# Kernel tuning notes

Hardware: AMD Instinct MI355X
Metric: run time of the kernel (lower is better)

Reference implementation:

```python
import jax, jax.numpy as jnp
import numpy as np

B, S, D, H, P, E, K, HID = 512, 32, 256, 4, 3, 8, 2, 1024


def setup_inputs() -> dict:
    key = jax.random.key(0)
    ks = jax.random.split(key, 24)
    g = lambda k, sh, sc=0.02: jax.random.normal(k, sh, jnp.float32) * sc
    return {
        'x': jax.random.normal(ks[0], (B, S, D), jnp.float32),
        'pos': jax.random.normal(ks[1], (B, S, P), jnp.float32),
        'ln1_w': jnp.ones((D,), jnp.float32), 'ln1_b': jnp.zeros((D,), jnp.float32),
        'ln2_w': jnp.ones((D,), jnp.float32), 'ln2_b': jnp.zeros((D,), jnp.float32),
        'q_w': g(ks[2], (D, D)), 'k_w': g(ks[3], (D, D)), 'v_w': g(ks[4], (D, D)),
        'p1_w': g(ks[5], (P, P), 0.3), 'p1_b': jnp.zeros((P,), jnp.float32),
        'p2_w': g(ks[6], (P, D // 8), 0.3), 'p2_b': jnp.zeros((D // 8,), jnp.float32),
        'head_w': g(ks[7], (D // 8, H), 0.1), 'head_b': jnp.zeros((H,), jnp.float32),
        'gate_p': jnp.ones((H,), jnp.float32),
        'out_w': g(ks[8], (D, D)), 'out_b': jnp.zeros((D,), jnp.float32),
        'w_gate': g(ks[9], (D, E), 0.1),
        'e_w1': g(ks[10], (E, D, HID)), 'e_b1': jnp.zeros((E, HID), jnp.float32),
        'e_w2': g(ks[11], (E, HID, D)), 'e_b2': jnp.zeros((E, D), jnp.float32),
    }


def _layer_norm(z, w, b):
    m = z.mean(-1, keepdims=True)
    v = ((z - m) ** 2).mean(-1, keepdims=True)
    return (z - m) * jax.lax.rsqrt(v + 1e-6) * w + b


def reference(x, pos, ln1_w, ln1_b, ln2_w, ln2_b, q_w, k_w, v_w,
              p1_w, p1_b, p2_w, p2_b, head_w, head_b, gate_p,
              out_w, out_b, w_gate, e_w1, e_b1, e_w2, e_b2):
    Bx, Sx, Dx = x.shape
    dh = Dx // H
    # --- gated attention (qk attn mixed with pos-relative attn) ---
    h = _layer_norm(x, ln1_w, ln1_b)
    q = (h @ q_w).reshape(Bx, Sx, H, dh).transpose(0, 2, 1, 3)
    k = (h @ k_w).reshape(Bx, Sx, H, dh).transpose(0, 2, 1, 3)
    v = (h @ v_w).reshape(Bx, Sx, H, dh).transpose(0, 2, 1, 3)
    attn = jax.nn.softmax(jnp.einsum('bhqd,bhkd->bhqk', q, k) / jnp.sqrt(jnp.float32(dh)), axis=-1)
    pf = jax.nn.relu(pos @ p1_w + p1_b) @ p2_w + p2_b          # [B,S,D//8]
    diff = pf[:, :, None, :] - pf[:, None, :, :]               # [B,S,S,D//8]
    pos_attn = jax.nn.softmax((diff @ head_w + head_b).transpose(0, 3, 1, 2), axis=-1)
    gsig = jax.nn.sigmoid(gate_p)[None, :, None, None]
    mix = (1.0 - gsig) * attn + gsig * pos_attn
    mix = mix / mix.sum(-1, keepdims=True)
    o = jnp.einsum('bhqk,bhkd->bhqd', mix, v).transpose(0, 2, 1, 3).reshape(Bx, Sx, Dx)
    x = x + (o @ out_w + out_b)
    # --- MoE FFN: noisy top-k gate (eval: no noise), dispatch, expert GEMM, combine ---
    h2 = _layer_norm(x, ln2_w, ln2_b)
    flat = h2.reshape(-1, Dx)                                   # [T,D]
    T = flat.shape[0]
    logits = flat @ w_gate                                      # [T,E]
    topv, topi = jax.lax.top_k(logits, K)
    gates = jax.nn.softmax(topv, axis=-1)                       # [T,K]
    C = 2 * T * K // E                                          # capacity factor 2 (effectively no drops)
    eidx = topi.reshape(-1)                                     # [T*K], token-major
    oh = jax.nn.one_hot(eidx, E, dtype=jnp.int32)
    posn = jnp.take_along_axis(jnp.cumsum(oh, axis=0) - 1, eidx[:, None], axis=1)[:, 0]
    keep = posn < C
    posc = jnp.where(keep, posn, 0)
    xd = jnp.repeat(flat, K, axis=0) * keep[:, None].astype(flat.dtype)
    buf = jnp.zeros((E, C, Dx), flat.dtype).at[eidx, posc].add(xd)   # grouped dispatch
    hh = jax.nn.gelu(jnp.einsum('ecd,edh->ech', buf, e_w1) + e_b1[:, None, :], approximate=False)
    y = jnp.einsum('ech,ehd->ecd', hh, e_w2) + e_b2[:, None, :]
    tok = y[eidx, posc] * (keep.astype(flat.dtype) * gates.reshape(-1))[:, None]
    moe_out = tok.reshape(T, K, Dx).sum(axis=1)
    return x + moe_out.reshape(Bx, Sx, Dx)
```

## Files before the change

### kernel.cpp

```cpp
#include <hip/hip_runtime.h>
#include <hip/hip_bf16.h>
#include <math.h>

#define BB 512
#define SS 32
#define DD 256
#define HH 4
#define DHH 64
#define PP 3
#define EE 8
#define KTOP 2
#define HID 1024
#define TT (BB*SS)
#define CAP 8192
#define TD ((size_t)TT*DD)

typedef short short8 __attribute__((ext_vector_type(8)));
typedef float f32x4 __attribute__((ext_vector_type(4)));

#define GLL(gp, lp) __builtin_amdgcn_global_load_lds( \
    (const __attribute__((address_space(1))) void*)(gp), \
    (__attribute__((address_space(3))) void*)(lp), 16, 0, 0)

__device__ __forceinline__ float wred(float v) {
#pragma unroll
  for (int off = 32; off; off >>= 1) v += __shfl_xor(v, off, 64);
  return v;
}

__device__ __forceinline__ float f4c(const float4& f, int u) {
  return (u == 0) ? f.x : (u == 1) ? f.y : (u == 2) ? f.z : f.w;
}

__device__ __forceinline__ unsigned short f2b(float f) {
  union { float f; unsigned u; } x; x.f = f;
  unsigned r = x.u + 0x7fffu + ((x.u >> 16) & 1u);
  return (unsigned short)(r >> 16);
}

__device__ __forceinline__ float b2f(unsigned short u) {
  union { unsigned u; float f; } x; x.u = ((unsigned)u) << 16;
  return x.f;
}

__device__ __forceinline__ unsigned cvt_pk_bf16(float lo, float hi) {
  unsigned r;
  asm("v_cvt_pk_bf16_f32 %0, %1, %2" : "=v"(r) : "v"(lo), "v"(hi));
  return r;
}

__device__ __forceinline__ float gelu_f(float x) {
  float x2 = x * x;
  float t2 = x * __builtin_fmaf(x2, 0.102943842f, 2.30212326f);
  float e = __builtin_amdgcn_exp2f(t2);
  float r = __builtin_amdgcn_rcpf(e + 1.f);
  float th = __builtin_fmaf(-2.f, r, 1.f);
  return 0.5f * x * (1.f + th);
}

__global__ void k_prep(
    const float* __restrict__ ew1, unsigned short* __restrict__ w1s,
    const float* __restrict__ ew2, unsigned short* __restrict__ w2s,
    const float* __restrict__ qw, const float* __restrict__ kw,
    const float* __restrict__ vw, unsigned short* __restrict__ wqkvf,
    const float* __restrict__ outw, unsigned short* __restrict__ woutf,
    const float* __restrict__ pos, const float* __restrict__ p1w,
    const float* __restrict__ p1b, const float* __restrict__ p2w,
    const float* __restrict__ p2b, const float* __restrict__ headw,
    float* __restrict__ pa,
    const float* __restrict__ x, const float* __restrict__ ln1w,
    const float* __restrict__ ln1b, unsigned short* __restrict__ rhi,
    unsigned short* __restrict__ rlo) {
  __shared__ float shbuf[2*HH*SS];
  int bid = blockIdx.x;
  int tid = threadIdx.x;
  if (bid < 2048) {
    const float* src = (bid < 1024) ? ew1 : ew2;
    unsigned short* dst = (bid < 1024) ? w1s : w2s;
    int K = (bid < 1024) ? DD : HID;
    int N = (bid < 1024) ? HID : DD;
    int idx = (bid & 1023) * 256 + tid;
    int lane = idx & 63;
    int tile = idx >> 6;
    int ntn = N >> 4;
    int ntk = K >> 5;
    int e = tile / (ntk * ntn);
    int rem = tile - e * (ntk * ntn);
    int kt = rem / ntn;
    int nt = rem - kt * ntn;
    int g = lane >> 4, c = lane & 15;
    const float* s = src + ((size_t)e * K + kt*32 + g*8) * N + nt*16 + c;
    short8 frag;
#pragma unroll
    for (int j = 0; j < 8; ++j) frag[j] = (short)f2b(s[(size_t)j * N]);
    reinterpret_cast<short8*>(dst)[(size_t)tile * 64 + lane] = frag;
  } else if (bid < 2144) {
    int tile = (bid - 2048) * 4 + (tid >> 6);
    int lane = tid & 63;
    int kt = tile / 48, nt = tile % 48;
    int c = lane & 15, g = lane >> 4;
    const float* W = (nt < 16) ? qw : (nt < 32) ? kw : vw;
    int col = (nt & 15) * 16 + c;
    const float* s = W + ((size_t)kt*32 + g*8)*DD + col;
    short8 hi, lo;
#pragma unroll
    for (int j = 0; j < 8; ++j) {
      float xx = s[(size_t)j * DD];
      unsigned short hb = f2b(xx);
      hi[j] = (short)hb;
      lo[j] = (short)f2b(xx - b2f(hb));
    }
    short8* d = reinterpret_cast<short8*>(wqkvf);
    d[(size_t)tile*128 + lane] = hi;
    d[(size_t)tile*128 + 64 + lane] = lo;
  } else if (bid < 2176) {
    int tile = (bid - 2144) * 4 + (tid >> 6);
    int lane = tid & 63;
    int kt = tile >> 4, nt = tile & 15;
    int c = lane & 15, g = lane >> 4;
    int col = nt * 16 + c;
    const float* s = outw + ((size_t)kt*32 + g*8)*DD + col;
    short8 hi, lo;
#pragma unroll
    for (int j = 0; j < 8; ++j) {
      float xx = s[(size_t)j * DD];
      unsigned short hb = f2b(xx);
      hi[j] = (short)hb;
      lo[j] = (short)f2b(xx - b2f(hb));
    }
    short8* d = reinterpret_cast<short8*>(woutf);
    d[(size_t)tile*128 + lane] = hi;
    d[(size_t)tile*128 + 64 + lane] = lo;
  } else if (bid < 2688) {
    int b = bid - 2176;
    float* ph = shbuf;
    float* ex = shbuf + HH*SS;
    if (tid < 128) {
      int s = tid >> 2, hd = tid & 3;
      const float* pp = pos + ((size_t)b * SS + s) * PP;
      float p0 = pp[0], p1 = pp[1], p2 = pp[2];
      float t0 = fmaxf(0.f, p0*p1w[0] + p1*p1w[3] + p2*p1w[6] + p1b[0]);
      float t1 = fmaxf(0.f, p0*p1w[1] + p1*p1w[4] + p2*p1w[7] + p1b[1]);
      float t2 = fmaxf(0.f, p0*p1w[2] + p1*p1w[5] + p2*p1w[8] + p1b[2]);
      float acc = 0.f;
#pragma unroll
      for (int c = 0; c < 32; ++c) {
        float pf = t0*p2w[c] + t1*p2w[32+c] + t2*p2w[64+c] + p2b[c];
        acc += pf * headw[c*4 + hd];
      }
      ph[hd*SS + s] = acc;
    }
    __syncthreads();
    if (tid < 4) {
      int h2 = tid;
      float mx = -1e30f;
      for (int j = 0; j < 32; ++j) mx = fmaxf(mx, -ph[h2*SS + j]);
      float sum = 0.f;
      for (int j = 0; j < 32; ++j) { float e = expf(-ph[h2*SS + j] - mx); ex[h2*SS + j] = e; sum += e; }
      float inv = 1.f / sum;
      for (int j = 0; j < 32; ++j) pa[((size_t)b*HH + h2)*SS + j] = ex[h2*SS + j] * inv;
    }
  } else {
    int t = (bid - 2688) * 4 + (tid >> 6);
    int lane = tid & 63;
    float4 xv = reinterpret_cast<const float4*>(x + (size_t)t * DD)[lane];
    float s1 = xv.x + xv.y + xv.z + xv.w;
    float s2 = xv.x*xv.x + xv.y*xv.y + xv.z*xv.z + xv.w*xv.w;
    s1 = wred(s1); s2 = wred(s2);
    float m = s1 * (1.f/256.f);
    float var = s2 * (1.f/256.f) - m*m;
    float rs = rsqrtf(var + 1e-6f);
    float4 wv = reinterpret_cast<const float4*>(ln1w)[lane];
    float4 bv = reinterpret_cast<const float4*>(ln1b)[lane];
    float4 o;
    o.x = (xv.x-m)*rs*wv.x + bv.x;
    o.y = (xv.y-m)*rs*wv.y + bv.y;
    o.z = (xv.z-m)*rs*wv.z + bv.z;
    o.w = (xv.w-m)*rs*wv.w + bv.w;
    ushort4 h4, l4;
    h4.x = f2b(o.x); l4.x = f2b(o.x - b2f(h4.x));
    h4.y = f2b(o.y); l4.y = f2b(o.y - b2f(h4.y));
    h4.z = f2b(o.z); l4.z = f2b(o.z - b2f(h4.z));
    h4.w = f2b(o.w); l4.w = f2b(o.w - b2f(h4.w));
    *reinterpret_cast<ushort4*>(rhi + (size_t)t * DD + lane*4) = h4;
    *reinterpret_cast<ushort4*>(rlo + (size_t)t * DD + lane*4) = l4;
  }
}

__global__ __launch_bounds__(512, 4) void k_qkvm(
    const unsigned short* __restrict__ hr, const unsigned short* __restrict__ lr,
    const unsigned short* __restrict__ wqkvf,
    float* __restrict__ q, float* __restrict__ k, float* __restrict__ v) {
  __shared__ short8 AF[2048];
  int tid = threadIdx.x, lane = tid & 63, w = tid >> 6;
  int c = lane & 15, g = lane >> 4;
#pragma unroll
  for (int i = 0; i < 4; ++i) {
    int comb = i*8 + w;
    int mt = comb >> 4, slot = comb & 15;
    int kt = slot & 7;
    const unsigned short* src = (slot < 8) ? hr : lr;
    const unsigned short* sp = src + ((size_t)(blockIdx.x*32 + mt*16 + c)*DD + kt*32 + g*8);
    GLL(sp, AF + comb*64);
  }
  const short8* wfv = reinterpret_cast<const short8*>(wqkvf);
  f32x4 acc[2][6] = {};
  __syncthreads();
#pragma unroll
  for (int kt = 0; kt < 8; ++kt) {
    short8 bh[6], bl[6];
#pragma unroll
    for (int n = 0; n < 6; ++n) {
      const short8* bp = wfv + ((size_t)kt*48 + w*6 + n)*128;
      bh[n] = bp[lane]; bl[n] = bp[64 + lane];
    }
    short8 ah[2], al[2];
#pragma unroll
    for (int mt = 0; mt < 2; ++mt) {
      ah[mt] = AF[(mt*16 + kt)*64 + lane];
      al[mt] = AF[(mt*16 + 8 + kt)*64 + lane];
    }
    __builtin_amdgcn_s_setprio(1);
#pragma unroll
    for (int n = 0; n < 6; ++n)
#pragma unroll
      for (int mt = 0; mt < 2; ++mt) {
        acc[mt][n] = __builtin_amdgcn_mfma_f32_16x16x32_bf16(ah[mt], bh[n], acc[mt][n], 0, 0, 0);
        acc[mt][n] = __builtin_amdgcn_mfma_f32_16x16x32_bf16(al[mt], bh[n], acc[mt][n], 0, 0, 0);
        acc[mt][n] = __builtin_amdgcn_mfma_f32_16x16x32_bf16(ah[mt], bl[n], acc[mt][n], 0, 0, 0);
      }
    __builtin_amdgcn_s_setprio(0);
  }
#pragma unroll
  for (int n = 0; n < 6; ++n) {
    int col = w*96 + n*16 + c;
    int wsel = col >> 8, cc = col & 255;
    int hd = cc >> 6, d2 = cc & 63;
    float* OUT = (wsel == 0) ? q : (wsel == 1) ? k : v;
#pragma unroll
    for (int mt = 0; mt < 2; ++mt) {
#pragma unroll
      for (int r = 0; r < 4; ++r) {
        int tok = (blockIdx.x*2 + mt)*16 + g*4 + r;
        int b = tok >> 5, s = tok & 31;
        OUT[(((size_t)b*HH + hd)*SS + s)*DHH + d2] = acc[mt][n][r];
      }
    }
  }
}

__global__ __launch_bounds__(512, 4) void k_outm(
    const unsigned short* __restrict__ hr, const unsigned short* __restrict__ lr,
    const unsigned short* __restrict__ wof,
    const float* __restrict__ xres, const float* __restrict__ bias,
    float* __restrict__ out) {
  __shared__ short8 AF[2048];
  int tid = threadIdx.x, lane = tid & 63, w = tid >> 6;
  int c = lane & 15, g = lane >> 4;
#pragma unroll
  for (int i = 0; i < 4; ++i) {
    int comb = i*8 + w;
    int mt = comb >> 4, slot = comb & 15;
    int kt = slot & 7;
    const unsigned short* src = (slot < 8) ? hr : lr;
    const unsigned short* sp = src + ((size_t)(blockIdx.x*32 + mt*16 + c)*DD + kt*32 + g*8);
    GLL(sp, AF + comb*64);
  }
  const short8* wfv = reinterpret_cast<const short8*>(wof);
  f32x4 acc[2][2] = {};
  __syncthreads();
#pragma unroll
  for (int kt = 0; kt < 8; ++kt) {
    short8 bh[2], bl[2];
#pragma unroll
    for (int n = 0; n < 2; ++n) {
      const short8* bp = wfv + ((size_t)kt*16 + w*2 + n)*128;
      bh[n] = bp[lane]; bl[n] = bp[64 + lane];
    }
    short8 ah[2], al[2];
#pragma unroll
    for (int mt = 0; mt < 2; ++mt) {
      ah[mt] = AF[(mt*16 + kt)*64 + lane];
      al[mt] = AF[(mt*16 + 8 + kt)*64 + lane];
    }
    __builtin_amdgcn_s_setprio(1);
#pragma unroll
    for (int n = 0; n < 2; ++n)
#pragma unroll
      for (int mt = 0; mt < 2; ++mt) {
        acc[mt][n] = __builtin_amdgcn_mfma_f32_16x16x32_bf16(ah[mt], bh[n], acc[mt][n], 0, 0, 0);
        acc[mt][n] = __builtin_amdgcn_mfma_f32_16x16x32_bf16(al[mt], bh[n], acc[mt][n], 0, 0, 0);
        acc[mt][n] = __builtin_amdgcn_mfma_f32_16x16x32_bf16(ah[mt], bl[n], acc[mt][n], 0, 0, 0);
      }
    __builtin_amdgcn_s_setprio(0);
  }
#pragma unroll
  for (int n = 0; n < 2; ++n) {
    int col = (w*2 + n)*16 + c;
    float bb = bias[col];
#pragma unroll
    for (int mt = 0; mt < 2; ++mt) {
#pragma unroll
      for (int r = 0; r < 4; ++r) {
        int tok = (blockIdx.x*2 + mt)*16 + g*4 + r;
        size_t idx = (size_t)tok*DD + col;
        out[idx] = xres[idx] + acc[mt][n][r] + bb;
      }
    }
  }
}

__global__ __launch_bounds__(256) void k_attn(const float* __restrict__ q, const float* __restrict__ k,
        const float* __restrict__ v, const float* __restrict__ pa, const float* __restrict__ gate_p,
        unsigned short* __restrict__ ahi, unsigned short* __restrict__ alo) {
  int bh = blockIdx.x;
  int b = bh >> 2, hd = bh & 3;
  __shared__ float qs[32][65];
  __shared__ float ks[32][65];
  __shared__ float vs[32][64];
  __shared__ float ssm[32][33];
  __shared__ float pas[32];
  int tid = threadIdx.x;
  const float* qb = q + (size_t)bh * (SS*DHH);
  const float* kb = k + (size_t)bh * (SS*DHH);
  const float* vb = v + (size_t)bh * (SS*DHH);
  for (int it = tid; it < 512; it += 256) {
    int row = it >> 4, col = (it & 15) * 4;
    float4 qv = *reinterpret_cast<const float4*>(qb + row*DHH + col);
    float4 kv = *reinterpret_cast<const float4*>(kb + row*DHH + col);
    float4 vv = *reinterpret_cast<const float4*>(vb + row*DHH + col);
    qs[row][col] = qv.x; qs[row][col+1] = qv.y; qs[row][col+2] = qv.z; qs[row][col+3] = qv.w;
    ks[row][col] = kv.x; ks[row][col+1] = kv.y; ks[row][col+2] = kv.z; ks[row][col+3] = kv.w;
    *reinterpret_cast<float4*>(&vs[row][col]) = vv;
  }
  if (tid < 32) pas[tid] = pa[(size_t)bh * SS + tid];
  __syncthreads();
#pragma unroll
  for (int rr = 0; rr < 4; ++rr) {
    int id = tid + 256*rr;
    int i = id >> 5, j = id & 31;
    float acc = 0.f;
#pragma unroll
    for (int d = 0; d < 64; ++d) acc += qs[i][d] * ks[j][d];
    ssm[i][j] = acc * 0.125f;
  }
  __syncthreads();
  float gs = 1.f / (1.f + expf(-gate_p[hd]));
  float ga = 1.f - gs;
  {
    int i = tid >> 3, sub = tid & 7;
    float v0 = ssm[i][sub*4+0], v1 = ssm[i][sub*4+1];
    float v2 = ssm[i][sub*4+2], v3 = ssm[i][sub*4+3];
    float mx = fmaxf(fmaxf(v0, v1), fmaxf(v2, v3));
#pragma unroll
    for (int off = 1; off < 8; off <<= 1) mx = fmaxf(mx, __shfl_xor(mx, off, 64));
    float e0 = expf(v0-mx), e1 = expf(v1-mx), e2 = expf(v2-mx), e3 = expf(v3-mx);
    float s = e0 + e1 + e2 + e3;
#pragma unroll
    for (int off = 1; off < 8; off <<= 1) s += __shfl_xor(s, off, 64);
    float inv = 1.f / s;
    ssm[i][sub*4+0] = ga*e0*inv + gs*pas[sub*4+0];
    ssm[i][sub*4+1] = ga*e1*inv + gs*pas[sub*4+1];
    ssm[i][sub*4+2] = ga*e2*inv + gs*pas[sub*4+2];
    ssm[i][sub*4+3] = ga*e3*inv + gs*pas[sub*4+3];
  }
  __syncthreads();
  {
    int w = tid >> 6, lane = tid & 63;
    int mt = w & 1, ktl = w >> 1;
    int c = lane & 15, g = lane >> 4;
    int tokl = mt*16 + c;
    int dbase = ktl*32 + g*8;
    float acc[8] = {};
#pragma unroll
    for (int j = 0; j < 32; ++j) {
      float s = ssm[tokl][j];
      float4 va = *reinterpret_cast<float4*>(&vs[j][dbase]);
      float4 vb2 = *reinterpret_cast<float4*>(&vs[j][dbase+4]);
      acc[0] += s*va.x;  acc[1] += s*va.y;  acc[2] += s*va.z;  acc[3] += s*va.w;
      acc[4] += s*vb2.x; acc[5] += s*vb2.y; acc[6] += s*vb2.z; acc[7] += s*vb2.w;
    }
    short8 hi, lo;
#pragma unroll
    for (int j = 0; j < 8; ++j) {
      unsigned short hb = f2b(acc[j]);
      hi[j] = (short)hb;
      lo[j] = (short)f2b(acc[j] - b2f(hb));
    }
    size_t base = ((size_t)(b*SS + tokl))*DD + hd*DHH + dbase;
    *reinterpret_cast<short8*>(ahi + base) = hi;
    *reinterpret_cast<short8*>(alo + base) = lo;
  }
}

__global__ void k_gate(const float* __restrict__ xo, const float* __restrict__ w,
                       const float* __restrict__ b, const float* __restrict__ wg,
                       unsigned short* __restrict__ flatb, int* __restrict__ topi,
                       float* __restrict__ gates) {
  int t = blockIdx.x * 4 + (threadIdx.x >> 6);
  int lane = threadIdx.x & 63;
  float4 xv = reinterpret_cast<const float4*>(xo + (size_t)t * DD)[lane];
  float s1 = xv.x + xv.y + xv.z + xv.w;
  float s2 = xv.x*xv.x + xv.y*xv.y + xv.z*xv.z + xv.w*xv.w;
  s1 = wred(s1); s2 = wred(s2);
  float m = s1 * (1.f/256.f);
  float var = s2 * (1.f/256.f) - m*m;
  float rs = rsqrtf(var + 1e-6f);
  float4 wv = reinterpret_cast<const float4*>(w)[lane];
  float4 bv = reinterpret_cast<const float4*>(b)[lane];
  float4 fv;
  fv.x = (xv.x-m)*rs*wv.x + bv.x;
  fv.y = (xv.y-m)*rs*wv.y + bv.y;
  fv.z = (xv.z-m)*rs*wv.z + bv.z;
  fv.w = (xv.w-m)*rs*wv.w + bv.w;
  ushort4 fb;
  fb.x = f2b(fv.x); fb.y = f2b(fv.y); fb.z = f2b(fv.z); fb.w = f2b(fv.w);
  *reinterpret_cast<ushort4*>(flatb + (size_t)t * DD + lane*4) = fb;
  float pe[8] = {};
  const float* wgp = wg + lane*4*EE;
#pragma unroll
  for (int dd = 0; dd < 4; ++dd) {
    float fd = f4c(fv, dd);
#pragma unroll
    for (int e2 = 0; e2 < 8; ++e2) pe[e2] += fd * wgp[dd*EE + e2];
  }
#pragma unroll
  for (int off = 32; off; off >>= 1) {
#pragma unroll
    for (int e2 = 0; e2 < 8; ++e2) pe[e2] += __shfl_xor(pe[e2], off, 64);
  }
  if (lane == 0) {
    float best = -1e30f, second = -1e30f; int bi = 0, si = 0;
#pragma unroll
    for (int e2 = 0; e2 < 8; ++e2) {
      float vv = pe[e2];
      if (vv > best) { second = best; si = bi; best = vv; bi = e2; }
      else if (vv > second) { second = vv; si = e2; }
    }
    float e1 = expf(second - best);
    float inv = 1.f / (1.f + e1);
    topi[t*2+0] = bi; topi[t*2+1] = si;
    gates[t*2+0] = inv; gates[t*2+1] = e1 * inv;
  }
}

__global__ void k_hist(const int* __restrict__ topi, int* __restrict__ bc) {
  __shared__ int cnt[EE];
  int tid = threadIdx.x;
  if (tid < EE) cnt[tid] = 0;
  __syncthreads();
  int e = topi[blockIdx.x*256 + tid];
  atomicAdd(&cnt[e], 1);
  __syncthreads();
  if (tid < EE) bc[blockIdx.x*EE + tid] = cnt[tid];
}

__global__ void k_disp(const int* __restrict__ topi, const int* __restrict__ bc,
                       int* __restrict__ ltok, int* __restrict__ slotof,
                       int* __restrict__ cnt) {
  __shared__ int offs[EE];
  __shared__ int wcnt[4][EE];
  int tid = threadIdx.x;
  {
    int e = tid >> 5, l32 = tid & 31;
    int sumP = 0, sumT = 0;
#pragma unroll
    for (int it = 0; it < 4; ++it) {
      int blk = l32 + it*32;
      int vv = bc[blk*EE + e];
      sumT += vv;
      if (blk < blockIdx.x) sumP += vv;
    }
#pragma unroll
    for (int off = 1; off < 32; off <<= 1) {
      sumP += __shfl_xor(sumP, off, 32);
      sumT += __shfl_xor(sumT, off, 32);
    }
    if (l32 == 0) {
      offs[e] = sumP;
      if (blockIdx.x == 0) cnt[e] = sumT;
    }
  }
  __syncthreads();
  int i = blockIdx.x*256 + tid;
  int e = topi[i];
  int wv = tid >> 6, lane = tid & 63;
  unsigned long long lt = (1ull << lane) - 1ull;
  int prefix = 0;
#pragma unroll
  for (int ee = 0; ee < EE; ++ee) {
    unsigned long long mb = __ballot(e == ee);
    if (e == ee) prefix = __popcll(mb & lt);
    if (lane == 0) wcnt[wv][ee] = __popcll(mb);
  }
  __syncthreads();
  int off = offs[e];
  for (int w2 = 0; w2 < wv; ++w2) off += wcnt[w2][e];
  int pos = off + prefix;
  if (pos < CAP) { ltok[e*CAP + pos] = i >> 1; slotof[i] = e*CAP + pos; }
  else           { slotof[i] = -1; }
}

__global__ __launch_bounds__(512, 4) void k_expert(
    const unsigned short* __restrict__ flatb, const unsigned short* __restrict__ w1s,
    const float* __restrict__ b1, const unsigned short* __restrict__ w2s,
    const float* __restrict__ b2,
    const int* __restrict__ ltok, const int* __restrict__ cnt,
    unsigned short* __restrict__ ybuf) {
  int e = blockIdx.x & 7;
  int rt0 = blockIdx.x >> 3;
  int kept = cnt[e]; if (kept > CAP) kept = CAP;
  int r0 = rt0 * 64;
  if (r0 >= kept) return;
  __shared__ short8 AsV[2048];
  __shared__ short8 H1V[2048];
  int tid = threadIdx.x;
  int lane = tid & 63;
  int w = tid >> 6;
  int c = lane & 15, g = lane >> 4;
  int ts = w & 1, dq = w >> 1;
  {
    const short8* fb = reinterpret_cast<const short8*>(flatb);
#pragma unroll
    for (int it = 0; it < 4; ++it) {
      int id = tid + it*512;
      int row = id >> 5, ch = id & 31;
      int rr = r0 + row;
      int src = (rr < kept) ? rr : r0;
      int tok = ltok[e*CAP + src];
      AsV[row*32 + (ch ^ (row & 7))] = fb[(size_t)tok*32 + ch];
    }
  }
  const short8* w1v = reinterpret_cast<const short8*>(w1s);
  const short8* w2v = reinterpret_cast<const short8*>(w2s);
  f32x4 y[2][4] = {};
  __syncthreads();
  for (int hc = 0; hc < 8; ++hc) {
    f32x4 hacc[4] = {};
    short8 wf[8];
#pragma unroll
    for (int kt = 0; kt < 8; ++kt)
      wf[kt] = w1v[((size_t)(e*8 + kt)*64 + hc*8 + w)*64 + lane];
#pragma unroll
    for (int kt = 0; kt < 8; ++kt) {
      __builtin_amdgcn_s_setprio(1);
#pragma unroll
      for (int ctT = 0; ctT < 4; ++ctT) {
        short8 a = AsV[(ctT*16 + c)*32 + ((kt*4 + g) ^ (c & 7))];
        hacc[ctT] = __builtin_amdgcn_mfma_f32_16x16x32_bf16(wf[kt], a, hacc[ctT], 0, 0, 0);
      }
      __builtin_amdgcn_s_setprio(0);
    }
    float4 b1v = *reinterpret_cast<const float4*>(b1 + e*HID + hc*128 + w*16 + g*4);
    {
      uint2* h1u = reinterpret_cast<uint2*>(H1V + (hc & 1)*1024);
#pragma unroll
      for (int ctT = 0; ctT < 4; ++ctT) {
        float v0 = gelu_f(hacc[ctT][0] + b1v.x);
        float v1 = gelu_f(hacc[ctT][1] + b1v.y);
        float v2 = gelu_f(hacc[ctT][2] + b1v.z);
        float v3 = gelu_f(hacc[ctT][3] + b1v.w);
        uint2 pk;
        pk.x = cvt_pk_bf16(v0, v1);
        pk.y = cvt_pk_bf16(v2, v3);
        int tok = ctT*16 + c;
        h1u[(tok*32 + w*4 + g) ^ ((c & 7) << 1)] = pk;
      }
    }
    __syncthreads();
#pragma unroll
    for (int hk = 0; hk < 4; ++hk) {
      short8 wg2[4];
#pragma unroll
      for (int ct = 0; ct < 4; ++ct)
        wg2[ct] = w2v[((size_t)(e*32 + hc*4 + hk)*16 + dq*4 + ct)*64 + lane];
      short8 a2[2];
#pragma unroll
      for (int rt = 0; rt < 2; ++rt) {
        int row = (ts*2 + rt)*16 + c;
        a2[rt] = H1V[(hc & 1)*1024 + row*16 + ((hk*4 + g) ^ (c & 7))];
      }
      __builtin_amdgcn_s_setprio(1);
#pragma unroll
      for (int ct = 0; ct < 4; ++ct)
#pragma unroll
        for (int rt = 0; rt < 2; ++rt)
          y[rt][ct] = __builtin_amdgcn_mfma_f32_16x16x32_bf16(a2[rt], wg2[ct], y[rt][ct], 0, 0, 0);
      __builtin_amdgcn_s_setprio(0);
    }
  }
  float bb2[4];
#pragma unroll
  for (int ct = 0; ct < 4; ++ct) bb2[ct] = b2[e*DD + (dq*4 + ct)*16 + c];
#pragma unroll
  for (int rt = 0; rt < 2; ++rt) {
#pragma unroll
    for (int q = 0; q < 4; ++q) {
      int tok = (ts*2 + rt)*16 + g*4 + q;
      if (r0 + tok < kept) {
        size_t base = (size_t)(e*CAP + r0 + tok) * DD;
#pragma unroll
        for (int ct = 0; ct < 4; ++ct) {
          int dd = (dq*4 + ct)*16 + c;
          ybuf[base + dd] = f2b(y[rt][ct][q] + bb2[ct]);
        }
      }
    }
  }
}

__global__ void k_comb(const unsigned short* __restrict__ ybuf, const int* __restrict__ slotof,
                       const float* __restrict__ gates, float* __restrict__ out) {
  int t = blockIdx.x * 4 + (threadIdx.x >> 6);
  int lane = threadIdx.x & 63;
  int s0 = slotof[t*2], s1 = slotof[t*2+1];
  float g0 = gates[t*2], g1 = gates[t*2+1];
  float4 o = reinterpret_cast<float4*>(out + (size_t)t*DD)[lane];
  if (s0 >= 0) {
    ushort4 a = reinterpret_cast<const ushort4*>(ybuf + (size_t)s0*DD)[lane];
    o.x += g0*b2f(a.x); o.y += g0*b2f(a.y); o.z += g0*b2f(a.z); o.w += g0*b2f(a.w);
  }
  if (s1 >= 0) {
    ushort4 a = reinterpret_cast<const ushort4*>(ybuf + (size_t)s1*DD)[lane];
    o.x += g1*b2f(a.x); o.y += g1*b2f(a.y); o.z += g1*b2f(a.z); o.w += g1*b2f(a.w);
  }
  reinterpret_cast<float4*>(out + (size_t)t*DD)[lane] = o;
}

extern "C" void kernel_launch(void* const* d_in, const int* in_sizes, int n_in,
                              void* d_out, int out_size, void* d_ws, size_t ws_size,
                              hipStream_t stream) {
  (void)in_sizes; (void)n_in; (void)out_size; (void)ws_size;
  const float* x    = (const float*)d_in[0];
  const float* pos  = (const float*)d_in[1];
  const float* ln1w = (const float*)d_in[2];
  const float* ln1b = (const float*)d_in[3];
  const float* ln2w = (const float*)d_in[4];
  const float* ln2b = (const float*)d_in[5];
  const float* qw   = (const float*)d_in[6];
  const float* kw   = (const float*)d_in[7];
  const float* vw   = (const float*)d_in[8];
  const float* p1w  = (const float*)d_in[9];
  const float* p1b  = (const float*)d_in[10];
  const float* p2w  = (const float*)d_in[11];
  const float* p2b  = (const float*)d_in[12];
  const float* headw= (const float*)d_in[13];
  const float* gatep= (const float*)d_in[15];
  const float* outw = (const float*)d_in[16];
  const float* outb = (const float*)d_in[17];
  const float* wg   = (const float*)d_in[18];
  const float* ew1  = (const float*)d_in[19];
  const float* eb1  = (const float*)d_in[20];
  const float* ew2  = (const float*)d_in[21];
  const float* eb2  = (const float*)d_in[22];
  float* out = (float*)d_out;

  float* wsf  = (float*)d_ws;
  unsigned short* rhi = (unsigned short*)wsf;
  unsigned short* rlo = rhi + TD;
  float* qb   = wsf + TD;
  float* kb   = wsf + 2*TD;
  float* vb   = wsf + 3*TD;
  unsigned short* ybuf = (unsigned short*)(wsf + TD);
  unsigned short* flatb = (unsigned short*)(wsf + 4*TD);
  unsigned short* w1s   = flatb + TD;
  unsigned short* w2s   = w1s + (size_t)EE*DD*HID;
  float* pa   = wsf + 5*TD;
  float* gates= pa + 65536;
  int* topi   = (int*)(gates + 32768);
  int* ltok   = topi + 32768;
  int* bc     = ltok + 65536;
  int* bo     = bc + 1024;
  int* cnt    = bo + 1024;
  int* slotof = cnt + 8;
  unsigned short* wqkvf = (unsigned short*)(wsf + 5*TD + (1<<20));
  unsigned short* woutf = wqkvf + 393216;

  k_prep<<<dim3(6784), dim3(256), 0, stream>>>(
      ew1, w1s, ew2, w2s, qw, kw, vw, wqkvf, outw, woutf,
      pos, p1w, p1b, p2w, p2b, headw, pa,
      x, ln1w, ln1b, rhi, rlo);
  k_qkvm<<<dim3(TT/32), dim3(512), 0, stream>>>(rhi, rlo, wqkvf, qb, kb, vb);
  k_attn<<<dim3(BB*HH), dim3(256), 0, stream>>>(qb, kb, vb, pa, gatep, rhi, rlo);
  k_outm<<<dim3(TT/32), dim3(512), 0, stream>>>(rhi, rlo, woutf, x, outb, out);
  k_gate<<<dim3(TT/4), dim3(256), 0, stream>>>(out, ln2w, ln2b, wg, flatb, topi, gates);
  k_hist<<<dim3(128), dim3(256), 0, stream>>>(topi, bc);
  k_disp<<<dim3(128), dim3(256), 0, stream>>>(topi, bc, ltok, slotof, cnt);
  k_expert<<<dim3(EE*128), dim3(512), 0, stream>>>(flatb, w1s, eb1, w2s, eb2,
                                                   ltok, cnt, ybuf);
  k_comb<<<dim3(TT/4), dim3(256), 0, stream>>>(ybuf, slotof, gates, out);
}
```

Before: 184.4 us.

## Halve expert row tile to 32 tokens and load activations into registers

The expert FFN kernel now handles 32 tokens per block instead of 64 and doubles the grid. It drops the shared-memory staging of gathered token activations and has each lane load its MFMA operand fragments straight from global memory into registers. The second GEMM's N split is remapped across the 8 waves, and the hidden buffer in shared memory is halved. The intent is more blocks, better balance for uneven expert counts, and less LDS traffic and fewer barriers. The cost is that expert weights are reloaded twice as often per token, which lowers weight reuse.

```diff
diff --git a/kernel.cpp b/kernel.cpp
--- a/kernel.cpp
+++ b/kernel.cpp
@@ -510,56 +510,52 @@
   int e = blockIdx.x & 7;
   int rt0 = blockIdx.x >> 3;
   int kept = cnt[e]; if (kept > CAP) kept = CAP;
-  int r0 = rt0 * 64;
+  int r0 = rt0 * 32;
   if (r0 >= kept) return;
-  __shared__ short8 AsV[2048];
-  __shared__ short8 H1V[2048];
+  __shared__ short8 H1V[1024];
   int tid = threadIdx.x;
   int lane = tid & 63;
   int w = tid >> 6;
   int c = lane & 15, g = lane >> 4;
-  int ts = w & 1, dq = w >> 1;
-  {
-    const short8* fb = reinterpret_cast<const short8*>(flatb);
-#pragma unroll
-    for (int it = 0; it < 4; ++it) {
-      int id = tid + it*512;
-      int row = id >> 5, ch = id & 31;
-      int rr = r0 + row;
-      int src = (rr < kept) ? rr : r0;
-      int tok = ltok[e*CAP + src];
-      AsV[row*32 + (ch ^ (row & 7))] = fb[(size_t)tok*32 + ch];
-    }
+  int rr0 = r0 + c, rr1 = r0 + 16 + c;
+  int t0 = ltok[e*CAP + ((rr0 < kept) ? rr0 : r0)];
+  int t1 = ltok[e*CAP + ((rr1 < kept) ? rr1 : r0)];
+  const short8* fb = reinterpret_cast<const short8*>(flatb);
+  short8 af0[8], af1[8];
+#pragma unroll
+  for (int kt = 0; kt < 8; ++kt) {
+    af0[kt] = fb[(size_t)t0*32 + kt*4 + g];
+    af1[kt] = fb[(size_t)t1*32 + kt*4 + g];
   }
   const short8* w1v = reinterpret_cast<const short8*>(w1s);
   const short8* w2v = reinterpret_cast<const short8*>(w2s);
-  f32x4 y[2][4] = {};
-  __syncthreads();
+  f32x4 y[2][2] = {};
   for (int hc = 0; hc < 8; ++hc) {
-    f32x4 hacc[4] = {};
-    short8 wf[8];
-#pragma unroll
-    for (int kt = 0; kt < 8; ++kt)
-      wf[kt] = w1v[((size_t)(e*8 + kt)*64 + hc*8 + w)*64 + lane];
-#pragma unroll
-    for (int kt = 0; kt < 8; ++kt) {
+    f32x4 hacc[2] = {};
+#pragma unroll
+    for (int half = 0; half < 2; ++half) {
+      short8 wf[4];
+#pragma unroll
+      for (int i = 0; i < 4; ++i)
+        wf[i] = w1v[((size_t)(e*8 + half*4 + i)*64 + hc*8 + w)*64 + lane];
       __builtin_amdgcn_s_setprio(1);
 #pragma unroll
-      for (int ctT = 0; ctT < 4; ++ctT) {
-        short8 a = AsV[(ctT*16 + c)*32 + ((kt*4 + g) ^ (c & 7))];
-        hacc[ctT] = __builtin_amdgcn_mfma_f32_16x16x32_bf16(wf[kt], a, hacc[ctT], 0, 0, 0);
+      for (int i = 0; i < 4; ++i) {
+        hacc[0] = __builtin_amdgcn_mfma_f32_16x16x32_bf16(wf[i], af0[half*4 + i], hacc[0], 0, 0, 0);
+        hacc[1] = __builtin_amdgcn_mfma_f32_16x16x32_bf16(wf[i], af1[half*4 + i], hacc[1], 0, 0, 0);
       }
       __builtin_amdgcn_s_setprio(0);
     }
     float4 b1v = *reinterpret_cast<const float4*>(b1 + e*HID + hc*128 + w*16 + g*4);
     {
-      uint2* h1u = reinterpret_cast<uint2*>(H1V + (hc & 1)*1024);
-#pragma unroll
-      for (int ctT = 0; ctT < 4; ++ctT) {
-        float v0 = gelu_f(hacc[ctT][0] + b1v.x);
-        float v1 = gelu_f(hacc[ctT][1] + b1v.y);
-        float v2 = gelu_f(hacc[ctT][2] + b1v.z);
-        float v3 = gelu_f(hacc[ctT][3] + b1v.w);
+      uint2* h1u = reinterpret_cast<uint2*>(H1V + (hc & 1)*512);
+#pragma unroll
+      for (int ctT = 0; ctT < 2; ++ctT) {
+        f32x4 hv = (ctT == 0) ? hacc[0] : hacc[1];
+        float v0 = gelu_f(hv[0] + b1v.x);
+        float v1 = gelu_f(hv[1] + b1v.y);
+        float v2 = gelu_f(hv[2] + b1v.z);
+        float v3 = gelu_f(hv[3] + b1v.w);
         uint2 pk;
         pk.x = cvt_pk_bf16(v0, v1);
         pk.y = cvt_pk_bf16(v2, v3);
@@ -570,39 +566,37 @@
     __syncthreads();
 #pragma unroll
     for (int hk = 0; hk < 4; ++hk) {
-      short8 wg2[4];
-#pragma unroll
-      for (int ct = 0; ct < 4; ++ct)
-        wg2[ct] = w2v[((size_t)(e*32 + hc*4 + hk)*16 + dq*4 + ct)*64 + lane];
+      short8 wg2[2];
+#pragma unroll
+      for (int n2 = 0; n2 < 2; ++n2)
+        wg2[n2] = w2v[((size_t)(e*32 + hc*4 + hk)*16 + w*2 + n2)*64 + lane];
       short8 a2[2];
 #pragma unroll
-      for (int rt = 0; rt < 2; ++rt) {
-        int row = (ts*2 + rt)*16 + c;
-        a2[rt] = H1V[(hc & 1)*1024 + row*16 + ((hk*4 + g) ^ (c & 7))];
-      }
+      for (int ctT = 0; ctT < 2; ++ctT)
+        a2[ctT] = H1V[(hc & 1)*512 + (ctT*16 + c)*16 + ((hk*4 + g) ^ (c & 7))];
       __builtin_amdgcn_s_setprio(1);
 #pragma unroll
-      for (int ct = 0; ct < 4; ++ct)
-#pragma unroll
-        for (int rt = 0; rt < 2; ++rt)
-          y[rt][ct] = __builtin_amdgcn_mfma_f32_16x16x32_bf16(a2[rt], wg2[ct], y[rt][ct], 0, 0, 0);
+      for (int n2 = 0; n2 < 2; ++n2)
+#pragma unroll
+        for (int ctT = 0; ctT < 2; ++ctT)
+          y[ctT][n2] = __builtin_amdgcn_mfma_f32_16x16x32_bf16(a2[ctT], wg2[n2], y[ctT][n2], 0, 0, 0);
       __builtin_amdgcn_s_setprio(0);
     }
   }
-  float bb2[4];
-#pragma unroll
-  for (int ct = 0; ct < 4; ++ct) bb2[ct] = b2[e*DD + (dq*4 + ct)*16 + c];
-#pragma unroll
-  for (int rt = 0; rt < 2; ++rt) {
+  float bb2[2];
+#pragma unroll
+  for (int n2 = 0; n2 < 2; ++n2) bb2[n2] = b2[e*DD + (w*2 + n2)*16 + c];
+#pragma unroll
+  for (int ctT = 0; ctT < 2; ++ctT) {
 #pragma unroll
     for (int q = 0; q < 4; ++q) {
-      int tok = (ts*2 + rt)*16 + g*4 + q;
+      int tok = ctT*16 + g*4 + q;
       if (r0 + tok < kept) {
         size_t base = (size_t)(e*CAP + r0 + tok) * DD;
 #pragma unroll
-        for (int ct = 0; ct < 4; ++ct) {
-          int dd = (dq*4 + ct)*16 + c;
-          ybuf[base + dd] = f2b(y[rt][ct][q] + bb2[ct]);
+        for (int n2 = 0; n2 < 2; ++n2) {
+          int dd = (w*2 + n2)*16 + c;
+          ybuf[base + dd] = f2b(y[ctT][n2][q] + bb2[n2]);
         }
       }
     }
@@ -686,7 +680,7 @@
   k_gate<<<dim3(TT/4), dim3(256), 0, stream>>>(out, ln2w, ln2b, wg, flatb, topi, gates);
   k_hist<<<dim3(128), dim3(256), 0, stream>>>(topi, bc);
   k_disp<<<dim3(128), dim3(256), 0, stream>>>(topi, bc, ltok, slotof, cnt);
-  k_expert<<<dim3(EE*128), dim3(512), 0, stream>>>(flatb, w1s, eb1, w2s, eb2,
+  k_expert<<<dim3(EE*256), dim3(512), 0, stream>>>(flatb, w1s, eb1, w2s, eb2,
                                                    ltok, cnt, ybuf);
   k_comb<<<dim3(TT/4), dim3(256), 0, stream>>>(ybuf, slotof, gates, out);
 }
```

Measured after the change: 219.3 us. 19.0% more time.

## Switch expert FFN to 32x32x16 MFMA with repacked expert weights

Applied to the files above, without the earlier changes.

Rewrites the MoE expert kernel to use 32x32x16 bf16 MFMA instead of 16x16x32. The expert weights are repacked in the prep kernel to match the new fragment layout. Hidden chunks grow to 256 columns per pass, which halves the outer-loop iterations. The second GEMM's weight loads are double-buffered. The larger MFMA tiles are meant to cut LDS operand reads and instruction count per FLOP, at the cost of more accumulator registers and a new LDS swizzle layout.

```diff
diff --git a/kernel.cpp b/kernel.cpp
--- a/kernel.cpp
+++ b/kernel.cpp
@@ -17,6 +17,7 @@
 
 typedef short short8 __attribute__((ext_vector_type(8)));
 typedef float f32x4 __attribute__((ext_vector_type(4)));
+typedef float f32x16 __attribute__((ext_vector_type(16)));
 
 #define GLL(gp, lp) __builtin_amdgcn_global_load_lds( \
     (const __attribute__((address_space(1))) void*)(gp), \
@@ -74,26 +75,32 @@
   __shared__ float shbuf[2*HH*SS];
   int bid = blockIdx.x;
   int tid = threadIdx.x;
-  if (bid < 2048) {
-    const float* src = (bid < 1024) ? ew1 : ew2;
-    unsigned short* dst = (bid < 1024) ? w1s : w2s;
-    int K = (bid < 1024) ? DD : HID;
-    int N = (bid < 1024) ? HID : DD;
-    int idx = (bid & 1023) * 256 + tid;
+  if (bid < 1024) {
+    int idx = bid * 256 + tid;
     int lane = idx & 63;
     int tile = idx >> 6;
-    int ntn = N >> 4;
-    int ntk = K >> 5;
-    int e = tile / (ntk * ntn);
-    int rem = tile - e * (ntk * ntn);
-    int kt = rem / ntn;
-    int nt = rem - kt * ntn;
-    int g = lane >> 4, c = lane & 15;
-    const float* s = src + ((size_t)e * K + kt*32 + g*8) * N + nt*16 + c;
+    int e = tile >> 9;
+    int rem = tile & 511;
+    int ht = rem >> 4, ks = rem & 15;
+    int l31 = lane & 31, lg = lane >> 5;
+    const float* s = ew1 + ((size_t)e*256 + ks*16 + lg*8) * 1024 + ht*32 + l31;
     short8 frag;
 #pragma unroll
-    for (int j = 0; j < 8; ++j) frag[j] = (short)f2b(s[(size_t)j * N]);
-    reinterpret_cast<short8*>(dst)[(size_t)tile * 64 + lane] = frag;
+    for (int j = 0; j < 8; ++j) frag[j] = (short)f2b(s[(size_t)j * 1024]);
+    reinterpret_cast<short8*>(w1s)[(size_t)tile * 64 + lane] = frag;
+  } else if (bid < 2048) {
+    int idx = (bid - 1024) * 256 + tid;
+    int lane = idx & 63;
+    int tile = idx >> 6;
+    int e = tile >> 9;
+    int rem = tile & 511;
+    int dt = rem >> 6, ks2g = rem & 63;
+    int l31 = lane & 31, lg = lane >> 5;
+    const float* s = ew2 + ((size_t)e*1024 + ks2g*16 + lg*8) * 256 + dt*32 + l31;
+    short8 frag;
+#pragma unroll
+    for (int j = 0; j < 8; ++j) frag[j] = (short)f2b(s[(size_t)j * 256]);
+    reinterpret_cast<short8*>(w2s)[(size_t)tile * 64 + lane] = frag;
   } else if (bid < 2144) {
     int tile = (bid - 2048) * 4 + (tid >> 6);
     int lane = tid & 63;
@@ -501,6 +508,8 @@
   else           { slotof[i] = -1; }
 }
 
+#define MFMA32(A, B, C) __builtin_amdgcn_mfma_f32_32x32x16_bf16(A, B, C, 0, 0, 0)
+
 __global__ __launch_bounds__(512, 4) void k_expert(
     const unsigned short* __restrict__ flatb, const unsigned short* __restrict__ w1s,
     const float* __restrict__ b1, const unsigned short* __restrict__ w2s,
@@ -517,8 +526,7 @@
   int tid = threadIdx.x;
   int lane = tid & 63;
   int w = tid >> 6;
-  int c = lane & 15, g = lane >> 4;
-  int ts = w & 1, dq = w >> 1;
+  int l31 = lane & 31, lg = lane >> 5;
   {
     const short8* fb = reinterpret_cast<const short8*>(flatb);
 #pragma unroll
@@ -533,78 +541,84 @@
   }
   const short8* w1v = reinterpret_cast<const short8*>(w1s);
   const short8* w2v = reinterpret_cast<const short8*>(w2s);
-  f32x4 y[2][4] = {};
-  __syncthreads();
-  for (int hc = 0; hc < 8; ++hc) {
-    f32x4 hacc[4] = {};
-    short8 wf[8];
-#pragma unroll
-    for (int kt = 0; kt < 8; ++kt)
-      wf[kt] = w1v[((size_t)(e*8 + kt)*64 + hc*8 + w)*64 + lane];
-#pragma unroll
-    for (int kt = 0; kt < 8; ++kt) {
+  f32x16 y0 = {}, y1 = {};
+  __syncthreads();
+  for (int hp = 0; hp < 4; ++hp) {
+    f32x16 hacc0 = {}, hacc1 = {};
+    int ht = hp*8 + w;
+#pragma unroll
+    for (int kb = 0; kb < 8; ++kb) {
+      short8 wf0 = w1v[(((size_t)e*32 + ht)*16 + kb*2 + 0)*64 + lane];
+      short8 wf1 = w1v[(((size_t)e*32 + ht)*16 + kb*2 + 1)*64 + lane];
       __builtin_amdgcn_s_setprio(1);
 #pragma unroll
-      for (int ctT = 0; ctT < 4; ++ctT) {
-        short8 a = AsV[(ctT*16 + c)*32 + ((kt*4 + g) ^ (c & 7))];
-        hacc[ctT] = __builtin_amdgcn_mfma_f32_16x16x32_bf16(wf[kt], a, hacc[ctT], 0, 0, 0);
+      for (int i = 0; i < 2; ++i) {
+        short8 wfc = i ? wf1 : wf0;
+        int kc = (kb*2 + i)*2 + lg;
+        short8 a0 = AsV[(l31)*32      + (kc ^ (l31 & 7))];
+        short8 a1 = AsV[(32 + l31)*32 + (kc ^ (l31 & 7))];
+        hacc0 = MFMA32(wfc, a0, hacc0);
+        hacc1 = MFMA32(wfc, a1, hacc1);
       }
       __builtin_amdgcn_s_setprio(0);
     }
-    float4 b1v = *reinterpret_cast<const float4*>(b1 + e*HID + hc*128 + w*16 + g*4);
     {
-      uint2* h1u = reinterpret_cast<uint2*>(H1V + (hc & 1)*1024);
-#pragma unroll
-      for (int ctT = 0; ctT < 4; ++ctT) {
-        float v0 = gelu_f(hacc[ctT][0] + b1v.x);
-        float v1 = gelu_f(hacc[ctT][1] + b1v.y);
-        float v2 = gelu_f(hacc[ctT][2] + b1v.z);
-        float v3 = gelu_f(hacc[ctT][3] + b1v.w);
-        uint2 pk;
-        pk.x = cvt_pk_bf16(v0, v1);
-        pk.y = cvt_pk_bf16(v2, v3);
-        int tok = ctT*16 + c;
-        h1u[(tok*32 + w*4 + g) ^ ((c & 7) << 1)] = pk;
-      }
-    }
-    __syncthreads();
-#pragma unroll
-    for (int hk = 0; hk < 4; ++hk) {
-      short8 wg2[4];
-#pragma unroll
-      for (int ct = 0; ct < 4; ++ct)
-        wg2[ct] = w2v[((size_t)(e*32 + hc*4 + hk)*16 + dq*4 + ct)*64 + lane];
-      short8 a2[2];
-#pragma unroll
-      for (int rt = 0; rt < 2; ++rt) {
-        int row = (ts*2 + rt)*16 + c;
-        a2[rt] = H1V[(hc & 1)*1024 + row*16 + ((hk*4 + g) ^ (c & 7))];
-      }
-      __builtin_amdgcn_s_setprio(1);
-#pragma unroll
-      for (int ct = 0; ct < 4; ++ct)
-#pragma unroll
-        for (int rt = 0; rt < 2; ++rt)
-          y[rt][ct] = __builtin_amdgcn_mfma_f32_16x16x32_bf16(a2[rt], wg2[ct], y[rt][ct], 0, 0, 0);
-      __builtin_amdgcn_s_setprio(0);
-    }
-  }
-  float bb2[4];
-#pragma unroll
-  for (int ct = 0; ct < 4; ++ct) bb2[ct] = b2[e*DD + (dq*4 + ct)*16 + c];
-#pragma unroll
-  for (int rt = 0; rt < 2; ++rt) {
-#pragma unroll
-    for (int q = 0; q < 4; ++q) {
-      int tok = (ts*2 + rt)*16 + g*4 + q;
-      if (r0 + tok < kept) {
-        size_t base = (size_t)(e*CAP + r0 + tok) * DD;
-#pragma unroll
-        for (int ct = 0; ct < 4; ++ct) {
-          int dd = (dq*4 + ct)*16 + c;
-          ybuf[base + dd] = f2b(y[rt][ct][q] + bb2[ct]);
+      uint2* h1u = reinterpret_cast<uint2*>(H1V);
+#pragma unroll
+      for (int qd = 0; qd < 4; ++qd) {
+        float4 bb = *reinterpret_cast<const float4*>(b1 + e*HID + hp*256 + w*32 + qd*8 + lg*4);
+        int chunk = w*4 + qd;
+        {
+          int tok = l31;
+          float v0 = gelu_f(hacc0[qd*4+0] + bb.x);
+          float v1 = gelu_f(hacc0[qd*4+1] + bb.y);
+          float v2 = gelu_f(hacc0[qd*4+2] + bb.z);
+          float v3 = gelu_f(hacc0[qd*4+3] + bb.w);
+          uint2 pk; pk.x = cvt_pk_bf16(v0, v1); pk.y = cvt_pk_bf16(v2, v3);
+          h1u[tok*64 + (chunk ^ (tok & 7))*2 + lg] = pk;
+        }
+        {
+          int tok = 32 + l31;
+          float v0 = gelu_f(hacc1[qd*4+0] + bb.x);
+          float v1 = gelu_f(hacc1[qd*4+1] + bb.y);
+          float v2 = gelu_f(hacc1[qd*4+2] + bb.z);
+          float v3 = gelu_f(hacc1[qd*4+3] + bb.w);
+          uint2 pk; pk.x = cvt_pk_bf16(v0, v1); pk.y = cvt_pk_bf16(v2, v3);
+          h1u[tok*64 + (chunk ^ (tok & 7))*2 + lg] = pk;
         }
       }
+    }
+    short8 wgr[2];
+    wgr[0] = w2v[(((size_t)e*8 + w)*64 + hp*16 + 0)*64 + lane];
+    __syncthreads();
+#pragma unroll
+    for (int ks2 = 0; ks2 < 16; ++ks2) {
+      if (ks2 < 15)
+        wgr[(ks2+1)&1] = w2v[(((size_t)e*8 + w)*64 + hp*16 + ks2 + 1)*64 + lane];
+      int kc = ks2*2 + lg;
+      short8 a0 = H1V[(l31)*32      + (kc ^ (l31 & 7))];
+      short8 a1 = H1V[(32 + l31)*32 + (kc ^ (l31 & 7))];
+      __builtin_amdgcn_s_setprio(1);
+      y0 = MFMA32(a0, wgr[ks2&1], y0);
+      y1 = MFMA32(a1, wgr[ks2&1], y1);
+      __builtin_amdgcn_s_setprio(0);
+    }
+    __syncthreads();
+  }
+  float bb2 = b2[e*DD + w*32 + l31];
+  int dd = w*32 + l31;
+#pragma unroll
+  for (int r = 0; r < 16; ++r) {
+    int trow = (r & 3) + 8*(r >> 2) + 4*lg;
+    {
+      int tok = trow;
+      if (r0 + tok < kept)
+        ybuf[(size_t)(e*CAP + r0 + tok)*DD + dd] = f2b(y0[r] + bb2);
+    }
+    {
+      int tok = 32 + trow;
+      if (r0 + tok < kept)
+        ybuf[(size_t)(e*CAP + r0 + tok)*DD + dd] = f2b(y1[r] + bb2);
     }
   }
 }
```

New measurement: 189.7 us. 1.03x slower.

## Widen MoE expert hidden chunk to 256 and double-buffer W2 fragment loads

Applied to the files above, without the earlier changes.

The expert FFN loop now handles 256 hidden units per iteration (4 iterations instead of 8). Each wave computes two 16-wide hidden tiles per A fragment read from LDS, so LDS A-reads and barrier rounds per hidden unit are halved. The H1 staging buffer becomes a single larger tile with a new swizzle and an extra barrier per iteration instead of ping-pong buffers. W2 fragments are software-prefetched one step ahead to hide global latency. The cost is higher register pressure (more accumulators and prefetch registers), which could reduce occupancy; the MFMA macro is cosmetic.

```diff
diff --git a/kernel.cpp b/kernel.cpp
--- a/kernel.cpp
+++ b/kernel.cpp
@@ -21,6 +21,8 @@
 #define GLL(gp, lp) __builtin_amdgcn_global_load_lds( \
     (const __attribute__((address_space(1))) void*)(gp), \
     (__attribute__((address_space(3))) void*)(lp), 16, 0, 0)
+
+#define MFMA16(A, B, C) __builtin_amdgcn_mfma_f32_16x16x32_bf16(A, B, C, 0, 0, 0)
 
 __device__ __forceinline__ float wred(float v) {
 #pragma unroll
@@ -225,9 +227,9 @@
     for (int n = 0; n < 6; ++n)
 #pragma unroll
       for (int mt = 0; mt < 2; ++mt) {
-        acc[mt][n] = __builtin_amdgcn_mfma_f32_16x16x32_bf16(ah[mt], bh[n], acc[mt][n], 0, 0, 0);
-        acc[mt][n] = __builtin_amdgcn_mfma_f32_16x16x32_bf16(al[mt], bh[n], acc[mt][n], 0, 0, 0);
-        acc[mt][n] = __builtin_amdgcn_mfma_f32_16x16x32_bf16(ah[mt], bl[n], acc[mt][n], 0, 0, 0);
+        acc[mt][n] = MFMA16(ah[mt], bh[n], acc[mt][n]);
+        acc[mt][n] = MFMA16(al[mt], bh[n], acc[mt][n]);
+        acc[mt][n] = MFMA16(ah[mt], bl[n], acc[mt][n]);
       }
     __builtin_amdgcn_s_setprio(0);
   }
@@ -288,9 +290,9 @@
     for (int n = 0; n < 2; ++n)
 #pragma unroll
       for (int mt = 0; mt < 2; ++mt) {
-        acc[mt][n] = __builtin_amdgcn_mfma_f32_16x16x32_bf16(ah[mt], bh[n], acc[mt][n], 0, 0, 0);
-        acc[mt][n] = __builtin_amdgcn_mfma_f32_16x16x32_bf16(al[mt], bh[n], acc[mt][n], 0, 0, 0);
-        acc[mt][n] = __builtin_amdgcn_mfma_f32_16x16x32_bf16(ah[mt], bl[n], acc[mt][n], 0, 0, 0);
+        acc[mt][n] = MFMA16(ah[mt], bh[n], acc[mt][n]);
+        acc[mt][n] = MFMA16(al[mt], bh[n], acc[mt][n]);
+        acc[mt][n] = MFMA16(ah[mt], bl[n], acc[mt][n]);
       }
     __builtin_amdgcn_s_setprio(0);
   }
@@ -535,59 +537,70 @@
   const short8* w2v = reinterpret_cast<const short8*>(w2s);
   f32x4 y[2][4] = {};
   __syncthreads();
-  for (int hc = 0; hc < 8; ++hc) {
-    f32x4 hacc[4] = {};
-    short8 wf[8];
-#pragma unroll
-    for (int kt = 0; kt < 8; ++kt)
-      wf[kt] = w1v[((size_t)(e*8 + kt)*64 + hc*8 + w)*64 + lane];
+  for (int hp = 0; hp < 4; ++hp) {
+    f32x4 hacc[4][2] = {};
+    int nt0 = hp*16 + w*2;
 #pragma unroll
     for (int kt = 0; kt < 8; ++kt) {
+      short8 wf0 = w1v[((size_t)(e*8 + kt)*64 + nt0)*64 + lane];
+      short8 wf1 = w1v[((size_t)(e*8 + kt)*64 + nt0 + 1)*64 + lane];
       __builtin_amdgcn_s_setprio(1);
 #pragma unroll
       for (int ctT = 0; ctT < 4; ++ctT) {
         short8 a = AsV[(ctT*16 + c)*32 + ((kt*4 + g) ^ (c & 7))];
-        hacc[ctT] = __builtin_amdgcn_mfma_f32_16x16x32_bf16(wf[kt], a, hacc[ctT], 0, 0, 0);
+        hacc[ctT][0] = MFMA16(wf0, a, hacc[ctT][0]);
+        hacc[ctT][1] = MFMA16(wf1, a, hacc[ctT][1]);
       }
       __builtin_amdgcn_s_setprio(0);
     }
-    float4 b1v = *reinterpret_cast<const float4*>(b1 + e*HID + hc*128 + w*16 + g*4);
     {
-      uint2* h1u = reinterpret_cast<uint2*>(H1V + (hc & 1)*1024);
-#pragma unroll
-      for (int ctT = 0; ctT < 4; ++ctT) {
-        float v0 = gelu_f(hacc[ctT][0] + b1v.x);
-        float v1 = gelu_f(hacc[ctT][1] + b1v.y);
-        float v2 = gelu_f(hacc[ctT][2] + b1v.z);
-        float v3 = gelu_f(hacc[ctT][3] + b1v.w);
-        uint2 pk;
-        pk.x = cvt_pk_bf16(v0, v1);
-        pk.y = cvt_pk_bf16(v2, v3);
-        int tok = ctT*16 + c;
-        h1u[(tok*32 + w*4 + g) ^ ((c & 7) << 1)] = pk;
-      }
-    }
+      uint2* h1u = reinterpret_cast<uint2*>(H1V);
+#pragma unroll
+      for (int n = 0; n < 2; ++n) {
+        float4 b1v = *reinterpret_cast<const float4*>(b1 + e*HID + (nt0 + n)*16 + g*4);
+        int chunk = (w*2 + n)*2 + (g >> 1);
+        int half = g & 1;
+#pragma unroll
+        for (int ctT = 0; ctT < 4; ++ctT) {
+          int tok = ctT*16 + c;
+          float v0 = gelu_f(hacc[ctT][n][0] + b1v.x);
+          float v1 = gelu_f(hacc[ctT][n][1] + b1v.y);
+          float v2 = gelu_f(hacc[ctT][n][2] + b1v.z);
+          float v3 = gelu_f(hacc[ctT][n][3] + b1v.w);
+          uint2 pk;
+          pk.x = cvt_pk_bf16(v0, v1);
+          pk.y = cvt_pk_bf16(v2, v3);
+          h1u[tok*64 + (chunk ^ (tok & 7))*2 + half] = pk;
+        }
+      }
+    }
+    short8 wg2r[2][4];
+#pragma unroll
+    for (int ct = 0; ct < 4; ++ct)
+      wg2r[0][ct] = w2v[((size_t)(e*32 + hp*8 + 0)*16 + dq*4 + ct)*64 + lane];
     __syncthreads();
 #pragma unroll
-    for (int hk = 0; hk < 4; ++hk) {
-      short8 wg2[4];
-#pragma unroll
-      for (int ct = 0; ct < 4; ++ct)
-        wg2[ct] = w2v[((size_t)(e*32 + hc*4 + hk)*16 + dq*4 + ct)*64 + lane];
+    for (int hk = 0; hk < 8; ++hk) {
+      if (hk < 7) {
+#pragma unroll
+        for (int ct = 0; ct < 4; ++ct)
+          wg2r[(hk+1)&1][ct] = w2v[((size_t)(e*32 + hp*8 + hk+1)*16 + dq*4 + ct)*64 + lane];
+      }
       short8 a2[2];
 #pragma unroll
       for (int rt = 0; rt < 2; ++rt) {
         int row = (ts*2 + rt)*16 + c;
-        a2[rt] = H1V[(hc & 1)*1024 + row*16 + ((hk*4 + g) ^ (c & 7))];
+        a2[rt] = H1V[row*32 + ((hk*4 + g) ^ (c & 7))];
       }
       __builtin_amdgcn_s_setprio(1);
 #pragma unroll
       for (int ct = 0; ct < 4; ++ct)
 #pragma unroll
         for (int rt = 0; rt < 2; ++rt)
-          y[rt][ct] = __builtin_amdgcn_mfma_f32_16x16x32_bf16(a2[rt], wg2[ct], y[rt][ct], 0, 0, 0);
+          y[rt][ct] = MFMA16(a2[rt], wg2r[hk&1][ct], y[rt][ct]);
       __builtin_amdgcn_s_setprio(0);
     }
+    __syncthreads();
   }
   float bb2[4];
 #pragma unroll
```

Result: slower. 192.9 us (+4.6%).
